# Kernel optimization log

Hardware: AMD Instinct MI355X
Metric: run time of the kernel (lower is better)

The kernel has to match this reference:

```python
import jax, jax.numpy as jnp
import numpy as np

GROUPS = 8
EPS = 1e-3  # Keras GroupNormalization default epsilon


def group_norm(x, gamma, beta):
    b, h, w, c = x.shape
    xr = x.reshape(b, h, w, GROUPS, c // GROUPS)
    mean = jnp.mean(xr, axis=(1, 2, 4), keepdims=True)
    var = jnp.var(xr, axis=(1, 2, 4), keepdims=True)
    xn = ((xr - mean) * jax.lax.rsqrt(var + EPS)).reshape(b, h, w, c)
    return xn * gamma + beta


def setup_inputs() -> dict:
    key = jax.random.key(0)
    ks = jax.random.split(key, 6)
    B, H, W, C = 4, 64, 64, 256
    std = C ** -0.5
    return {
        "x": jax.random.normal(ks[0], (B, H, W, C), dtype=jnp.float32),
        "gamma": jnp.ones((C,), jnp.float32),
        "beta": jnp.zeros((C,), jnp.float32),
        "wq": jax.random.normal(ks[1], (C, C), jnp.float32) * std,
        "bq": jnp.zeros((C,), jnp.float32),
        "wk": jax.random.normal(ks[2], (C, C), jnp.float32) * std,
        "bk": jnp.zeros((C,), jnp.float32),
        "wv": jax.random.normal(ks[3], (C, C), jnp.float32) * std,
        "bv": jnp.zeros((C,), jnp.float32),
        "wp": jax.random.normal(ks[4], (C, C), jnp.float32) * std,
        "bp": jnp.zeros((C,), jnp.float32),
    }


def reference(x, gamma, beta, wq, bq, wk, bk, wv, bv, wp, bp):
    b, h, w, c = x.shape
    scale = jnp.asarray(c, x.dtype) ** -0.5
    xn = group_norm(x, gamma, beta)
    # 1x1 convs are per-pixel dense layers
    q = (xn @ wq + bq).reshape(b, h * w, c)
    k = (xn @ wk + bk).reshape(b, h * w, c)
    v = (xn @ wv + bv).reshape(b, h * w, c)
    scores = jnp.einsum('bic,bjc->bij', q, k) * scale  # [b, N, N]
    attn = jax.nn.softmax(scores, axis=-1)
    out = jnp.einsum('bij,bjc->bic', attn, v).reshape(b, h, w, c)
    return x + (out @ wp + bp)
```

## Files before the change

### kernel.cpp

```cpp
#include <hip/hip_runtime.h>

#define N_TOK 4096
#define C_DIM 256
#define BATCH 4
#define M_ROWS (BATCH * N_TOK)
#define GN_CNT 131072.0f

typedef __attribute__((ext_vector_type(4))) float f32x4;
typedef __attribute__((ext_vector_type(16))) float f32x16;
typedef __attribute__((ext_vector_type(8))) short s16x8;
typedef __attribute__((ext_vector_type(4))) unsigned short u16x4;
typedef __attribute__((ext_vector_type(4))) unsigned int u32x4;

static __device__ __forceinline__ unsigned short f2bf(float f) {
  unsigned int u = __builtin_bit_cast(unsigned int, f);
  u += 0x7fff + ((u >> 16) & 1);
  return (unsigned short)(u >> 16);
}
static __device__ __forceinline__ float bf2f(unsigned short h) {
  unsigned int u = ((unsigned int)h) << 16;
  return __builtin_bit_cast(float, u);
}

static __device__ __forceinline__ void gload_lds16(const void* g, void* l) {
  __builtin_amdgcn_global_load_lds(
      (__attribute__((address_space(1))) void*)(unsigned long long)(const char*)g,
      (__attribute__((address_space(3))) void*)l, 16, 0, 0);
}

__global__ __launch_bounds__(256) void prep(const float* __restrict__ x,
                                            const float* __restrict__ wq,
                                            const float* __restrict__ wk,
                                            const float* __restrict__ wv,
                                            const float* __restrict__ wp,
                                            float* __restrict__ partials,
                                            unsigned short* __restrict__ wT) {
  int tid = threadIdx.x;
  if (blockIdx.x < 512) {
    int bg = blockIdx.x >> 4, chunk = blockIdx.x & 15;
    int b = bg >> 3, g = bg & 7;
    const f32x4* x4 = (const f32x4*)x;
    float s1 = 0.f, s2 = 0.f;
#pragma unroll
    for (int it = 0; it < 8; ++it) {
      int idx = it * 256 + tid;
      int nl = idx >> 3, cq = idx & 7;
      f32x4 v = x4[(b * N_TOK + chunk * 256 + nl) * 64 + g * 8 + cq];
      s1 += v[0] + v[1] + v[2] + v[3];
      s2 += v[0] * v[0] + v[1] * v[1] + v[2] * v[2] + v[3] * v[3];
    }
    for (int m = 1; m < 64; m <<= 1) {
      s1 += __shfl_xor(s1, m, 64);
      s2 += __shfl_xor(s2, m, 64);
    }
    __shared__ float r1[4], r2[4];
    int wave = tid >> 6, lane = tid & 63;
    if (lane == 0) { r1[wave] = s1; r2[wave] = s2; }
    __syncthreads();
    if (tid == 0) {
      int slot = (bg * 16 + chunk) * 2;
      partials[slot]     = r1[0] + r1[1] + r1[2] + r1[3];
      partials[slot + 1] = r2[0] + r2[1] + r2[2] + r2[3];
    }
  } else {
    int rem = blockIdx.x - 512;
    int z = rem >> 6, t = rem & 63;
    int k0 = (t >> 3) * 32, n0 = (t & 7) * 32;
    const float* const srcs[4] = {wq, wk, wv, wp};
    const float* w = srcs[z];
    unsigned short* o = wT + z * 65536;
    __shared__ float tt[32][33];
    int tx = tid & 31, ty = tid >> 5;
#pragma unroll
    for (int ky = 0; ky < 32; ky += 8)
      tt[ty + ky][tx] = w[(k0 + ty + ky) * C_DIM + n0 + tx];
    __syncthreads();
#pragma unroll
    for (int ky = 0; ky < 32; ky += 8)
      o[(n0 + ty + ky) * C_DIM + k0 + tx] = f2bf(tt[tx][ty + ky]);
  }
}

__global__ __launch_bounds__(256, 2) void qkv_gemm(const float* __restrict__ x,
                                                   const unsigned short* __restrict__ wT,
                                                   const float* __restrict__ partials,
                                                   const float* __restrict__ gamma,
                                                   const float* __restrict__ beta,
                                                   const float* __restrict__ bq,
                                                   const float* __restrict__ bk,
                                                   const float* __restrict__ bv,
                                                   unsigned short* __restrict__ qo,
                                                   unsigned short* __restrict__ ko,
                                                   unsigned short* __restrict__ vo) {
  int tid = threadIdx.x;
  int wave = tid >> 6, lane = tid & 63, n32 = lane & 31, half = lane >> 5;
  int rg = wave >> 1, cv = wave & 1;
  int row0 = blockIdx.x * 64 + rg * 32;
  int c0 = blockIdx.y * 128;
  int row = row0 + n32;
  int batch = blockIdx.x >> 6;
  __shared__ __align__(16) unsigned short Wt[32768];
  __shared__ float mean_s[8], rstd_s[8];

#pragma unroll
  for (int ii = 0; ii < 32; ++ii) {
    int u = ii * 256 + tid;
    int n = u >> 5, ku = u & 31;
    gload_lds16(wT + (size_t)(c0 + n) * C_DIM + ((ku ^ (n & 7)) * 8), Wt + u * 8);
  }
  if (tid < 8) {
    const float* p = partials + (batch * 8 + tid) * 32;
    float s1 = 0.f, s2 = 0.f;
#pragma unroll
    for (int c = 0; c < 16; ++c) { s1 += p[2 * c]; s2 += p[2 * c + 1]; }
    float inv = 1.f / GN_CNT;
    float m = s1 * inv, v = s2 * inv - m * m;
    mean_s[tid] = m;
    rstd_s[tid] = rsqrtf(v + 1e-3f);
  }
  __syncthreads();

  float mean[8], rstd[8];
#pragma unroll
  for (int g = 0; g < 8; ++g) { mean[g] = mean_s[g]; rstd[g] = rstd_s[g]; }
  s16x8 af[16];
#pragma unroll
  for (int ks = 0; ks < 16; ++ks) {
    int cb = ks * 16 + half * 8;
    const f32x4* xp = (const f32x4*)(x + (size_t)row * C_DIM + cb);
    f32x4 v0 = xp[0], v1 = xp[1];
    const f32x4* g4 = (const f32x4*)(gamma + cb);
    const f32x4* b4 = (const f32x4*)(beta + cb);
    f32x4 ga0 = g4[0], ga1 = g4[1], be0 = b4[0], be1 = b4[1];
    int g = (2 * ks + half) >> 2;
    float m = mean[g], rs = rstd[g];
    s16x8 o;
#pragma unroll
    for (int j = 0; j < 4; ++j) {
      o[j]     = (short)f2bf((v0[j] - m) * rs * ga0[j] + be0[j]);
      o[4 + j] = (short)f2bf((v1[j] - m) * rs * ga1[j] + be1[j]);
    }
    af[ks] = o;
  }

  for (int w = 0; w < 3; ++w) {
    if (w > 0) {
      __syncthreads();
#pragma unroll
      for (int ii = 0; ii < 32; ++ii) {
        int u = ii * 256 + tid;
        int n = u >> 5, ku = u & 31;
        gload_lds16(wT + (size_t)w * 65536 + (size_t)(c0 + n) * C_DIM + ((ku ^ (n & 7)) * 8),
                    Wt + u * 8);
      }
      __syncthreads();
    }
    const float* bias = (w == 0) ? bq : (w == 1) ? bk : bv;
    unsigned short* outp = (w == 0) ? qo : (w == 1) ? ko : vo;
    float scale = (w == 0) ? 0.0625f : 1.f;
#pragma unroll
    for (int ct = 0; ct < 2; ++ct) {
      int nl = (cv * 2 + ct) * 32 + n32;
      f32x16 acc = (f32x16)(bias[c0 + nl]);
#pragma unroll
      for (int ks = 0; ks < 16; ++ks) {
        s16x8 wf = *(const s16x8*)(Wt + nl * C_DIM + (((2 * ks + half) ^ (nl & 7)) * 8));
        acc = __builtin_amdgcn_mfma_f32_32x32x16_bf16(af[ks], wf, acc, 0, 0, 0);
      }
#pragma unroll
      for (int r = 0; r < 16; ++r) {
        int rr = (r & 3) + 8 * (r >> 2) + 4 * half;
        outp[(size_t)(row0 + rr) * C_DIM + c0 + nl] = f2bf(acc[r] * scale);
      }
    }
  }
}

__global__ __launch_bounds__(256) void vtrans(const unsigned short* __restrict__ v,
                                              unsigned short* __restrict__ vT) {
  __shared__ unsigned short t[32][36];
  int n0 = blockIdx.x * 32, c0 = blockIdx.y * 32, b = blockIdx.z;
  int tid = threadIdx.x;
  int n = tid >> 3, c4 = (tid & 7) * 4;
  *(u16x4*)&t[n][c4] =
      *(const u16x4*)&v[((size_t)(b * N_TOK + n0 + n)) * C_DIM + c0 + c4];
  __syncthreads();
  int c = tid >> 3, n4 = (tid & 7) * 4;
  u16x4 o = {t[n4][c], t[n4 + 1][c], t[n4 + 2][c], t[n4 + 3][c]};
  *(u16x4*)&vT[((size_t)(b * C_DIM + c0 + c)) * N_TOK + n0 + n4] = o;
}

static __device__ __forceinline__ void stage_K(unsigned short* dst,
                                               const unsigned short* kb,
                                               int jbase, int tid) {
#pragma unroll
  for (int ii = 0; ii < 4; ++ii) {
    int u = ii * 256 + tid;
    int ksu = u >> 6, tok = (u >> 1) & 31, hf = u & 1;
    gload_lds16(kb + (size_t)(jbase + tok) * C_DIM + ksu * 16 + hf * 8, dst + u * 8);
  }
}
static __device__ __forceinline__ void stage_V(unsigned short* dst,
                                               const unsigned short* vb,
                                               int jbase, int tid) {
#pragma unroll
  for (int ii = 0; ii < 4; ++ii)
    gload_lds16(vb + (size_t)tid * N_TOK + jbase + ii * 8, dst + (ii * 256 + tid) * 8);
}

static __device__ __forceinline__ f32x16 qk_compute(const unsigned short* KT,
                                                    const s16x8* qf,
                                                    int n32, int half) {
  f32x16 sc = (f32x16)(0.f);
#pragma unroll
  for (int ks = 0; ks < 16; ++ks) {
    s16x8 kf = *(const s16x8*)(KT + ks * 512 + (n32 * 2 + half) * 8);
    sc = __builtin_amdgcn_mfma_f32_32x32x16_bf16(kf, qf[ks], sc, 0, 0, 0);
  }
  return sc;
}

__global__ __launch_bounds__(256, 2) void attn_part(const unsigned short* __restrict__ q,
                                                    const unsigned short* __restrict__ k,
                                                    const unsigned short* __restrict__ vT,
                                                    unsigned short* __restrict__ op0,
                                                    unsigned short* __restrict__ op1,
                                                    unsigned short* __restrict__ op2,
                                                    unsigned short* __restrict__ op3,
                                                    float* __restrict__ lbuf) {
  int tid = threadIdx.x;
  int wave = tid >> 6, lane = tid & 63;
  int n32 = lane & 31, half = lane >> 5;
  int i = blockIdx.x;
  int batch = (i >> 1) & 3;
  int slot = ((i >> 3) << 1) | (i & 1);
  int qb = slot & 31, chunk = slot >> 5;
  int qrow0 = batch * N_TOK + qb * 128 + wave * 32;
  const unsigned short* kb = k + (size_t)batch * N_TOK * C_DIM;
  const unsigned short* vb = vT + (size_t)batch * C_DIM * N_TOK;
  unsigned short* op = (chunk == 0) ? op0 : (chunk == 1) ? op1 : (chunk == 2) ? op2 : op3;

  __shared__ __align__(16) unsigned short K_lds[2][8192];
  __shared__ __align__(16) unsigned short V_lds[3][8192];

  int jbase0 = chunk * 1024;
  stage_K(K_lds[0], kb, jbase0, tid);
  stage_V(V_lds[0], vb, jbase0, tid);

  const unsigned short* qp = q + (size_t)(qrow0 + n32) * C_DIM;
  s16x8 qf[16];
#pragma unroll
  for (int ks = 0; ks < 16; ++ks)
    qf[ks] = *(const s16x8*)(qp + ks * 16 + half * 8);

  f32x16 Oa[8];
#pragma unroll
  for (int ct = 0; ct < 8; ++ct) Oa[ct] = (f32x16)(0.f);
  float ls = 0.f;

  __syncthreads();

  stage_K(K_lds[1], kb, jbase0 + 32, tid);
  stage_V(V_lds[1], vb, jbase0 + 32, tid);

  s16x8 pf0p, pf1p;
  {
    f32x16 sc = qk_compute(K_lds[0], qf, n32, half);
    unsigned D[8], E[8];
#pragma unroll
    for (int t = 0; t < 8; ++t) {
      float pa = exp2f(fmaf(sc[2 * t],     1.44269504f, -11.54156032f));
      float pb = exp2f(fmaf(sc[2 * t + 1], 1.44269504f, -11.54156032f));
      ls += pa + pb;
      D[t] = (__builtin_bit_cast(unsigned, pa) >> 16) |
             (__builtin_bit_cast(unsigned, pb) & 0xFFFF0000u);
      E[t] = __shfl_xor(D[t], 32);
    }
    u32x4 w0 = {half ? E[2] : D[0], half ? E[3] : D[1],
                half ? D[2] : E[0], half ? D[3] : E[1]};
    u32x4 w1 = {half ? E[6] : D[4], half ? E[7] : D[5],
                half ? D[6] : E[4], half ? D[7] : E[5]};
    pf0p = __builtin_bit_cast(s16x8, w0);
    pf1p = __builtin_bit_cast(s16x8, w1);
  }

  int vr_i = 0, vw_i = 2;
  for (int jt = 1; jt < 32; ++jt) {
    __syncthreads();
    if (jt < 31) {
      int jb2 = jbase0 + (jt + 1) * 32;
      stage_K(K_lds[(jt + 1) & 1], kb, jb2, tid);
      stage_V(V_lds[vw_i], vb, jb2, tid);
    }
    __builtin_amdgcn_s_setprio(1);
    f32x16 sc = qk_compute(K_lds[jt & 1], qf, n32, half);

    const unsigned short* VR = V_lds[vr_i];
    unsigned D[8], E[8];
#pragma unroll
    for (int t = 0; t < 8; ++t) {
      float pa = exp2f(fmaf(sc[2 * t],     1.44269504f, -11.54156032f));
      float pb = exp2f(fmaf(sc[2 * t + 1], 1.44269504f, -11.54156032f));
      ls += pa + pb;
      D[t] = (__builtin_bit_cast(unsigned, pa) >> 16) |
             (__builtin_bit_cast(unsigned, pb) & 0xFFFF0000u);
      E[t] = __shfl_xor(D[t], 32);
      int ch = t * 32 + n32;
      s16x8 vf0 = *(const s16x8*)(VR + (half * 256 + ch) * 8);
      s16x8 vf1 = *(const s16x8*)(VR + ((2 + half) * 256 + ch) * 8);
      Oa[t] = __builtin_amdgcn_mfma_f32_32x32x16_bf16(pf0p, vf0, Oa[t], 0, 0, 0);
      Oa[t] = __builtin_amdgcn_mfma_f32_32x32x16_bf16(pf1p, vf1, Oa[t], 0, 0, 0);
    }
    __builtin_amdgcn_s_setprio(0);

    u32x4 w0 = {half ? E[2] : D[0], half ? E[3] : D[1],
                half ? D[2] : E[0], half ? D[3] : E[1]};
    u32x4 w1 = {half ? E[6] : D[4], half ? E[7] : D[5],
                half ? D[6] : E[4], half ? D[7] : E[5]};
    pf0p = __builtin_bit_cast(s16x8, w0);
    pf1p = __builtin_bit_cast(s16x8, w1);
    vr_i = (vr_i == 2) ? 0 : vr_i + 1;
    vw_i = (vw_i == 2) ? 0 : vw_i + 1;
  }

  {
    const unsigned short* VR = V_lds[vr_i];
#pragma unroll
    for (int t = 0; t < 8; ++t) {
      int ch = t * 32 + n32;
      s16x8 vf0 = *(const s16x8*)(VR + (half * 256 + ch) * 8);
      s16x8 vf1 = *(const s16x8*)(VR + ((2 + half) * 256 + ch) * 8);
      Oa[t] = __builtin_amdgcn_mfma_f32_32x32x16_bf16(pf0p, vf0, Oa[t], 0, 0, 0);
      Oa[t] = __builtin_amdgcn_mfma_f32_32x32x16_bf16(pf1p, vf1, Oa[t], 0, 0, 0);
    }
  }

#pragma unroll
  for (int ct = 0; ct < 8; ++ct)
#pragma unroll
    for (int r = 0; r < 16; ++r) {
      int row = (r & 3) + 8 * (r >> 2) + 4 * half;
      op[(size_t)(qrow0 + row) * C_DIM + ct * 32 + n32] = f2bf(Oa[ct][r]);
    }
  float tot = ls + __shfl_xor(ls, 32);
  if (half == 0) lbuf[chunk * M_ROWS + qrow0 + n32] = tot;
}

__global__ __launch_bounds__(256, 2) void proj_gemm(const unsigned short* __restrict__ p0,
                                                    const unsigned short* __restrict__ p1,
                                                    const unsigned short* __restrict__ p2,
                                                    const unsigned short* __restrict__ p3,
                                                    const float* __restrict__ lbuf,
                                                    const unsigned short* __restrict__ wt,
                                                    const float* __restrict__ bp,
                                                    const float* __restrict__ x,
                                                    float* __restrict__ out) {
  int tid = threadIdx.x;
  int wave = tid >> 6, lane = tid & 63, n32 = lane & 31, half = lane >> 5;
  int rg = wave >> 1, cv = wave & 1;
  int row0 = blockIdx.x * 64 + rg * 32;
  int c0 = blockIdx.y * 128;
  __shared__ __align__(16) unsigned short Wt[32768];

#pragma unroll
  for (int ii = 0; ii < 32; ++ii) {
    int u = ii * 256 + tid;
    int n = u >> 5, ku = u & 31;
    gload_lds16(wt + (size_t)(c0 + n) * C_DIM + ((ku ^ (n & 7)) * 8), Wt + u * 8);
  }

  int row = row0 + n32;
  float linv = 1.f / (lbuf[row] + lbuf[M_ROWS + row] +
                      lbuf[2 * M_ROWS + row] + lbuf[3 * M_ROWS + row]);
  s16x8 af[16];
#pragma unroll
  for (int ks = 0; ks < 16; ++ks) {
    size_t off = (size_t)row * C_DIM + ks * 16 + half * 8;
    s16x8 a0 = *(const s16x8*)(p0 + off);
    s16x8 a1 = *(const s16x8*)(p1 + off);
    s16x8 a2 = *(const s16x8*)(p2 + off);
    s16x8 a3 = *(const s16x8*)(p3 + off);
    s16x8 o;
#pragma unroll
    for (int j = 0; j < 8; ++j) {
      float f = bf2f((unsigned short)a0[j]) + bf2f((unsigned short)a1[j]) +
                bf2f((unsigned short)a2[j]) + bf2f((unsigned short)a3[j]);
      o[j] = (short)f2bf(f * linv);
    }
    af[ks] = o;
  }
  __syncthreads();

#pragma unroll
  for (int ct = 0; ct < 2; ++ct) {
    int nl = (cv * 2 + ct) * 32 + n32;
    f32x16 acc = (f32x16)(bp[c0 + nl]);
#pragma unroll
    for (int ks = 0; ks < 16; ++ks) {
      s16x8 wf = *(const s16x8*)(Wt + nl * C_DIM + (((2 * ks + half) ^ (nl & 7)) * 8));
      acc = __builtin_amdgcn_mfma_f32_32x32x16_bf16(af[ks], wf, acc, 0, 0, 0);
    }
#pragma unroll
    for (int r = 0; r < 16; ++r) {
      int rr = (r & 3) + 8 * (r >> 2) + 4 * half;
      size_t idx = (size_t)(row0 + rr) * C_DIM + c0 + nl;
      out[idx] = acc[r] + x[idx];
    }
  }
}

extern "C" void kernel_launch(void* const* d_in, const int* in_sizes, int n_in,
                              void* d_out, int out_size, void* d_ws, size_t ws_size,
                              hipStream_t stream) {
  const float* x     = (const float*)d_in[0];
  const float* gamma = (const float*)d_in[1];
  const float* beta  = (const float*)d_in[2];
  const float* wq    = (const float*)d_in[3];
  const float* bq    = (const float*)d_in[4];
  const float* wk    = (const float*)d_in[5];
  const float* bk    = (const float*)d_in[6];
  const float* wv    = (const float*)d_in[7];
  const float* bv    = (const float*)d_in[8];
  const float* wp    = (const float*)d_in[9];
  const float* bp    = (const float*)d_in[10];
  float* out = (float*)d_out;

  char* ws = (char*)d_ws;
  const size_t MC = (size_t)M_ROWS * C_DIM;
  float* partials      = (float*)ws;
  unsigned short* wT   = (unsigned short*)(ws + 4096);
  unsigned short* qb   = wT + 4 * 65536;
  unsigned short* kbuf = qb + MC;
  unsigned short* vb   = kbuf + MC;
  unsigned short* vTb  = vb + MC;
  unsigned short* pl0  = vTb + MC;
  unsigned short* pl2  = pl0 + MC;
  unsigned short* pl3  = pl2 + MC;
  float* lbuf          = (float*)(pl3 + MC);
  unsigned short* pl1  = vb;

  prep<<<768, 256, 0, stream>>>(x, wq, wk, wv, wp, partials, wT);
  qkv_gemm<<<dim3(256, 2), 256, 0, stream>>>(x, wT, partials, gamma, beta,
                                             bq, bk, bv, qb, kbuf, vb);
  vtrans<<<dim3(128, 8, 4), 256, 0, stream>>>(vb, vTb);
  attn_part<<<512, 256, 0, stream>>>(qb, kbuf, vTb, pl0, pl1, pl2, pl3, lbuf);
  proj_gemm<<<dim3(256, 2), 256, 0, stream>>>(pl0, pl1, pl2, pl3, lbuf,
                                              wT + 3 * 65536, bp, x, out);
}
```

Baseline: 227.4 us.

## Fuse V transpose into QKV GEMM epilogue and reorder K staging layout

```diff
diff --git a/kernel.cpp b/kernel.cpp
--- a/kernel.cpp
+++ b/kernel.cpp
@@ -91,7 +91,7 @@
                                                    const float* __restrict__ bv,
                                                    unsigned short* __restrict__ qo,
                                                    unsigned short* __restrict__ ko,
-                                                   unsigned short* __restrict__ vo) {
+                                                   unsigned short* __restrict__ vTo) {
   int tid = threadIdx.x;
   int wave = tid >> 6, lane = tid & 63, n32 = lane & 31, half = lane >> 5;
   int rg = wave >> 1, cv = wave & 1;
@@ -143,6 +143,7 @@
     af[ks] = o;
   }
 
+  f32x16 vacc[2];
   for (int w = 0; w < 3; ++w) {
     if (w > 0) {
       __syncthreads();
@@ -156,7 +157,7 @@
       __syncthreads();
     }
     const float* bias = (w == 0) ? bq : (w == 1) ? bk : bv;
-    unsigned short* outp = (w == 0) ? qo : (w == 1) ? ko : vo;
+    unsigned short* outp = (w == 0) ? qo : ko;
     float scale = (w == 0) ? 0.0625f : 1.f;
 #pragma unroll
     for (int ct = 0; ct < 2; ++ct) {
@@ -167,27 +168,40 @@
         s16x8 wf = *(const s16x8*)(Wt + nl * C_DIM + (((2 * ks + half) ^ (nl & 7)) * 8));
         acc = __builtin_amdgcn_mfma_f32_32x32x16_bf16(af[ks], wf, acc, 0, 0, 0);
       }
-#pragma unroll
-      for (int r = 0; r < 16; ++r) {
-        int rr = (r & 3) + 8 * (r >> 2) + 4 * half;
-        outp[(size_t)(row0 + rr) * C_DIM + c0 + nl] = f2bf(acc[r] * scale);
+      if (w < 2) {
+#pragma unroll
+        for (int r = 0; r < 16; ++r) {
+          int rr = (r & 3) + 8 * (r >> 2) + 4 * half;
+          outp[(size_t)(row0 + rr) * C_DIM + c0 + nl] = f2bf(acc[r] * scale);
+        }
+      } else {
+        vacc[ct] = acc;
       }
     }
   }
-}
-
-__global__ __launch_bounds__(256) void vtrans(const unsigned short* __restrict__ v,
-                                              unsigned short* __restrict__ vT) {
-  __shared__ unsigned short t[32][36];
-  int n0 = blockIdx.x * 32, c0 = blockIdx.y * 32, b = blockIdx.z;
-  int tid = threadIdx.x;
-  int n = tid >> 3, c4 = (tid & 7) * 4;
-  *(u16x4*)&t[n][c4] =
-      *(const u16x4*)&v[((size_t)(b * N_TOK + n0 + n)) * C_DIM + c0 + c4];
+
   __syncthreads();
-  int c = tid >> 3, n4 = (tid & 7) * 4;
-  u16x4 o = {t[n4][c], t[n4 + 1][c], t[n4 + 2][c], t[n4 + 3][c]};
-  *(u16x4*)&vT[((size_t)(b * C_DIM + c0 + c)) * N_TOK + n0 + n4] = o;
+#pragma unroll
+  for (int ct = 0; ct < 2; ++ct) {
+    int ch = (cv * 2 + ct) * 32 + n32;
+#pragma unroll
+    for (int g = 0; g < 4; ++g) {
+      u16x4 pk;
+#pragma unroll
+      for (int j = 0; j < 4; ++j) pk[j] = f2bf(vacc[ct][g * 4 + j]);
+      int tok = rg * 32 + 8 * g + 4 * half;
+      *(u16x4*)&Wt[ch * 72 + tok] = pk;
+    }
+  }
+  __syncthreads();
+  {
+    int ch = tid >> 1, nh = tid & 1;
+    int tokb = (blockIdx.x & 63) * 64;
+    const u32x4* srcp = (const u32x4*)&Wt[ch * 72 + nh * 32];
+    u32x4* dstp = (u32x4*)&vTo[((size_t)(batch * C_DIM + c0 + ch)) * N_TOK + tokb + nh * 32];
+#pragma unroll
+    for (int qq = 0; qq < 4; ++qq) dstp[qq] = srcp[qq];
+  }
 }
 
 static __device__ __forceinline__ void stage_K(unsigned short* dst,
@@ -196,7 +210,7 @@
 #pragma unroll
   for (int ii = 0; ii < 4; ++ii) {
     int u = ii * 256 + tid;
-    int ksu = u >> 6, tok = (u >> 1) & 31, hf = u & 1;
+    int ksu = u >> 6, hf = (u >> 5) & 1, tok = u & 31;
     gload_lds16(kb + (size_t)(jbase + tok) * C_DIM + ksu * 16 + hf * 8, dst + u * 8);
   }
 }
@@ -214,7 +228,7 @@
   f32x16 sc = (f32x16)(0.f);
 #pragma unroll
   for (int ks = 0; ks < 16; ++ks) {
-    s16x8 kf = *(const s16x8*)(KT + ks * 512 + (n32 * 2 + half) * 8);
+    s16x8 kf = *(const s16x8*)(KT + ks * 512 + (half * 32 + n32) * 8);
     sc = __builtin_amdgcn_mfma_f32_32x32x16_bf16(kf, qf[ks], sc, 0, 0, 0);
   }
   return sc;
@@ -441,8 +455,7 @@
 
   prep<<<768, 256, 0, stream>>>(x, wq, wk, wv, wp, partials, wT);
   qkv_gemm<<<dim3(256, 2), 256, 0, stream>>>(x, wT, partials, gamma, beta,
-                                             bq, bk, bv, qb, kbuf, vb);
-  vtrans<<<dim3(128, 8, 4), 256, 0, stream>>>(vb, vTb);
+                                             bq, bk, bv, qb, kbuf, vTb);
   attn_part<<<512, 256, 0, stream>>>(qb, kbuf, vTb, pl0, pl1, pl2, pl3, lbuf);
   proj_gemm<<<dim3(256, 2), 256, 0, stream>>>(pl0, pl1, pl2, pl3, lbuf,
                                               wT + 3 * 65536, bp, x, out);
```

Measured after the change: 232.9 us. 2.4% more time.
